# Kernel optimization log

Measured on AMD Instinct MI355X. Metric: run time of the kernel, lower is better.

## Reference

```python
import jax, jax.numpy as jnp
import numpy as np

# ---- static config (from init_kwargs) ----
SAMPLE_RATE = 2048.0
MAX_SHIFT = int(0.025 * SAMPLE_RATE)          # 51 samples
NUM_BINS = 16
FFTLENGTH = 1.0                               # chisq_kernel_length (s)
DF = 1.0 / FFTLENGTH
NUM_FREQS = int(FFTLENGTH * SAMPLE_RATE // 2 + 1)   # 1025 == rfft bins of 2048 samples
HIGHPASS = 32.0
CHISQ_PENALTY = 1.0
_freqs = np.arange(NUM_FREQS) / FFTLENGTH
MASK = _freqs >= HIGHPASS                     # static numpy bool mask

BATCH, CHANNELS, DIM = 256, 2, 2048


def setup_inputs() -> dict:
    key = jax.random.key(0)
    k1, k2 = jax.random.split(key)
    x_hat = jax.random.normal(k1, (BATCH, CHANNELS, DIM), dtype=jnp.float32)
    x = jax.random.normal(k2, (BATCH, CHANNELS, DIM), dtype=jnp.float32)
    return {"x_hat": x_hat, "x": x}


def _center(x):
    xmin = x.min(-1, keepdims=True)
    xmax = x.max(-1, keepdims=True)
    return 2 * (x - xmin) / (xmax - xmin) - 1


def _shifted_pearson(x, y, max_shift):
    # x, y: [B, C, T]; returns corr: [W, B, C] with W = 2*max_shift + 1
    b, c, t = x.shape
    num_windows = 2 * max_shift + 1
    xp = jnp.pad(x, ((0, 0), (0, 0), (max_shift, max_shift)))
    # window w, position i -> xp[..., i + w]  (same layout as torch unfold)
    idx = jnp.arange(num_windows)[:, None] + jnp.arange(t)[None, :]   # [W, T]
    xw = xp[:, :, idx]                                                # [B, C, W, T]
    xw = jnp.transpose(xw, (2, 0, 1, 3))                              # [W, B, C, T]
    xw = xw - xw.mean(-1, keepdims=True)
    yc = y - y.mean(-1, keepdims=True)
    corr = (xw * yc).sum(-1)
    norm = (xw ** 2).sum(-1) * (yc ** 2).sum(-1)
    return corr / jnp.sqrt(norm)


def _snr_integral(a, b):
    # |4 * a * conj(b) * df| cumulatively summed over frequency
    integrand = a * jnp.conj(b)
    return jnp.abs(4 * integrand * DF).cumsum(-1)


def _chisq(htilde, stilde):
    htilde = htilde[:, :, MASK]
    stilde = stilde[:, :, MASK]
    # partition frequencies by the template's own optimal-SNR integral
    si = _snr_integral(htilde, htilde)                    # [B, C, F]
    total = si[:, :, -1:]
    bins = (jnp.arange(NUM_BINS + 1, dtype=si.dtype) / NUM_BINS) * total  # [B, C, NB+1]
    search = jax.vmap(jax.vmap(lambda a, v: jnp.searchsorted(a, v, side="right")))
    edges = search(si, bins)
    edges = jnp.clip(edges, 0, si.shape[-1] - 1)
    qtilde = htilde / jnp.sqrt(total).astype(htilde.dtype)
    # SNR per bin of the normalized template against the strain
    si2 = _snr_integral(qtilde, stilde)                   # [B, C, F]
    total2 = si2[:, :, -1:]
    right = jnp.take_along_axis(si2, edges[:, :, 1:], axis=-1)
    left = jnp.take_along_axis(si2, edges[:, :, :-1], axis=-1)
    snr_per_bin = right - left                            # [B, C, NB]
    summand = (snr_per_bin - total2 / NUM_BINS) ** 2
    chisq = NUM_BINS * summand.sum(-1) / (NUM_BINS - 1)
    return total2[:, :, 0], chisq


def reference(x_hat, x):
    x_hat = _center(x_hat)
    corr = _shifted_pearson(x_hat, x, MAX_SHIFT)          # [W, B, C]
    corr = corr.max(0)                                    # [B, C]
    loss = (1 - corr) / (1 + corr)
    htilde = jnp.fft.rfft(x_hat, axis=-1) / SAMPLE_RATE   # [B, C, 1025] complex
    stilde = jnp.fft.rfft(x, axis=-1) / SAMPLE_RATE
    _, chisq = _chisq(htilde, stilde)
    chisq = chisq * CHISQ_PENALTY
    loss = loss * (1 + chisq ** 3) ** (1.0 / 6.0)
    return loss
```

## Files before the change

kernel.cpp:

```cpp
#include <hip/hip_runtime.h>
#include <math.h>

#define ROWS 512
#define DIM 2048
#define MS 51
#define NWIN 103
#define KMIN 32
#define NMASK 993
#define PHYS(i) ((i) + ((i) >> 5))

__global__ __launch_bounds__(256) void fused_mfl_kernel(
    const float* __restrict__ xhat, const float* __restrict__ x,
    float* __restrict__ out)
{
    const int r = blockIdx.x;
    const int t = threadIdx.x;
    const int lane = t & 63;
    const int wave = t >> 6;
    const float* xh = xhat + (size_t)r * DIM;
    const float* xr = x + (size_t)r * DIM;

    __shared__ float smem[9216];
    float* yh    = smem;
    float* yc    = smem + 2224;
    float* headS = smem + 4352;
    float* headQ = smem + 4404;
    float* tailS = smem + 4456;
    float* tailQ = smem + 4508;
    float2* A  = (float2*)smem;
    float2* Bb = (float2*)(smem + 4096);
    float2* TW = (float2*)(smem + 8192);
    float* siA = smem + 4096;
    float* siB = smem + 5120;

    __shared__ float red[32];
    __shared__ float sc[8];
    __shared__ int   edges[17];
    __shared__ float summ[16];
    __shared__ float wsum[4];

    float4 a0 = ((const float4*)xh)[2 * t];
    float4 a1 = ((const float4*)xh)[2 * t + 1];
    float4 b0 = ((const float4*)xr)[2 * t];
    float4 b1 = ((const float4*)xr)[2 * t + 1];
    float av[8] = {a0.x, a0.y, a0.z, a0.w, a1.x, a1.y, a1.z, a1.w};
    float bv[8] = {b0.x, b0.y, b0.z, b0.w, b1.x, b1.y, b1.z, b1.w};

#pragma unroll
    for (int k = 0; k < 2; ++k) {
        int u = t + 256 * k;
        float swv, cwv;
        sincosf((float)u * (-3.14159265358979323846f / 1024.0f), &swv, &cwv);
        TW[u] = make_float2(cwv, swv);
    }

    float mn = av[0], mx = av[0], sx = 0.f;
#pragma unroll
    for (int j = 0; j < 8; ++j) {
        mn = fminf(mn, av[j]); mx = fmaxf(mx, av[j]); sx += bv[j];
    }
#pragma unroll
    for (int d = 32; d; d >>= 1) {
        mn = fminf(mn, __shfl_down(mn, d));
        mx = fmaxf(mx, __shfl_down(mx, d));
        sx += __shfl_down(sx, d);
    }
    if (lane == 0) { red[wave] = mn; red[8 + wave] = mx; red[16 + wave] = sx; }
    __syncthreads();
    if (t == 0) {
        sc[0] = fminf(fminf(red[0], red[1]), fminf(red[2], red[3]));
        sc[1] = fmaxf(fmaxf(red[8], red[9]), fmaxf(red[10], red[11]));
        sc[2] = (red[16] + red[17] + red[18] + red[19]) * (1.0f / DIM);
    }
    __syncthreads();
    mn = sc[0]; mx = sc[1];
    const float mean = sc[2];
    const float scale = 2.0f / (mx - mn);

    float s1 = 0.f, s2 = 0.f, syy = 0.f;
    float yhv[8];
#pragma unroll
    for (int j = 0; j < 8; ++j) {
        float y = (av[j] - mn) * scale - 1.0f;
        float z = bv[j] - mean;
        yhv[j] = y;
        s1 += y; s2 += y * y; syy += z * z;
        int i = 8 * t + j;
        yh[PHYS(i + MS)] = y;
        yc[PHYS(i)] = z;
    }
    if (t < MS) { yh[PHYS(t)] = 0.f; yh[PHYS(t + MS + DIM)] = 0.f; }

#pragma unroll
    for (int d = 32; d; d >>= 1) {
        s1 += __shfl_down(s1, d); s2 += __shfl_down(s2, d); syy += __shfl_down(syy, d);
    }
    if (lane == 0) { red[wave] = s1; red[8 + wave] = s2; red[16 + wave] = syy; }
    __syncthreads();
    if (t == 0) {
        sc[3] = red[0] + red[1] + red[2] + red[3];
        sc[4] = red[8] + red[9] + red[10] + red[11];
        sc[5] = red[16] + red[17] + red[18] + red[19];
    }
    __syncthreads();
    const float S1 = sc[3], S2 = sc[4], Syy = sc[5];

    if (wave < 2) {
        float v = 0.f;
        if (lane >= 1 && lane <= MS)
            v = (wave == 0) ? yh[PHYS(MS + lane - 1)] : yh[PHYS(MS + DIM - lane)];
        float s = v, q = v * v;
#pragma unroll
        for (int d = 1; d < 64; d <<= 1) {
            float ys = __shfl_up(s, d);
            float yq = __shfl_up(q, d);
            if (lane >= d) { s += ys; q += yq; }
        }
        if (lane <= MS) {
            if (wave == 0) { headS[lane] = s; headQ[lane] = q; }
            else           { tailS[lane] = s; tailQ[lane] = q; }
        }
    }
    __syncthreads();

    float ycr[32];
#pragma unroll
    for (int j = 0; j < 32; ++j) ycr[j] = yc[PHYS(32 * lane + j)];

    const int c0 = 26 * wave;
    const int base0 = 32 * lane + c0;
    float wreg[32];
#pragma unroll
    for (int j = 0; j < 32; ++j) wreg[j] = yh[PHYS(base0 + j)];

    float cmax = -2.0f;
#pragma unroll
    for (int i = 0; i < 26; ++i) {
        float acc = 0.f;
#pragma unroll
        for (int j = 0; j < 32; ++j) acc += wreg[(i + j) & 31] * ycr[j];
#pragma unroll
        for (int d = 32; d; d >>= 1) acc += __shfl_down(acc, d);
        int c = c0 + i;
        if (lane == 0 && c < NWIN) {
            int off = c - MS;
            float sw, qw;
            if (off >= 0) { sw = S1 - headS[off]; qw = S2 - headQ[off]; }
            else          { sw = S1 - tailS[-off]; qw = S2 - tailQ[-off]; }
            float varw = qw - sw * sw * (1.0f / DIM);
            float corr = acc / sqrtf(varw * Syy);
            cmax = fmaxf(cmax, corr);
        }
        if (i < 25) wreg[i & 31] = yh[PHYS(base0 + 32 + i)];
    }
    if (lane == 0) red[wave] = cmax;
    __syncthreads();
    if (t == 0) {
        float m = fmaxf(fmaxf(red[0], red[1]), fmaxf(red[2], red[3]));
        sc[6] = (1.0f - m) / (1.0f + m);
    }
    __syncthreads();

#pragma unroll
    for (int j = 0; j < 8; ++j) {
        A[8 * t + j] = make_float2(yhv[j], bv[j]);
    }
    __syncthreads();

    float2 *S = A, *D = Bb;
#pragma unroll
    for (int stage = 0; stage < 5; ++stage) {
        const int s = 1 << (2 * stage);
#pragma unroll
        for (int k = 0; k < 2; ++k) {
            int q = t + 256 * k;
            int u = q & ~(s - 1);
            float2 x0 = S[q];
            float2 x1 = S[q + 512];
            float2 x2 = S[q + 1024];
            float2 x3 = S[q + 1536];
            float t0r = x0.x + x2.x, t0i = x0.y + x2.y;
            float t1r = x0.x - x2.x, t1i = x0.y - x2.y;
            float t2r = x1.x + x3.x, t2i = x1.y + x3.y;
            float d3r = x1.x - x3.x, d3i = x1.y - x3.y;
            float t3r = d3i, t3i = -d3r;
            float2 w1 = TW[u];
            float w2r = w1.x * w1.x - w1.y * w1.y, w2i = 2.f * w1.x * w1.y;
            float w3r = w2r * w1.x - w2i * w1.y,  w3i = w2r * w1.y + w2i * w1.x;
            float y0r = t0r + t2r, y0i = t0i + t2i;
            float a1r = t1r + t3r, a1i = t1i + t3i;
            float y1r = a1r * w1.x - a1i * w1.y, y1i = a1r * w1.y + a1i * w1.x;
            float a2r = t0r - t2r, a2i = t0i - t2i;
            float y2r = a2r * w2r - a2i * w2i, y2i = a2r * w2i + a2i * w2r;
            float a3r = t1r - t3r, a3i = t1i - t3i;
            float y3r = a3r * w3r - a3i * w3i, y3i = a3r * w3i + a3i * w3r;
            int base = q + 3 * u;
            D[base]         = make_float2(y0r, y0i);
            D[base + s]     = make_float2(y1r, y1i);
            D[base + 2 * s] = make_float2(y2r, y2i);
            D[base + 3 * s] = make_float2(y3r, y3i);
        }
        __syncthreads();
        float2* tmp = S; S = D; D = tmp;
    }
#pragma unroll
    for (int k = 0; k < 4; ++k) {
        int b = t + 256 * k;
        float2 a = S[b], c = S[b + 1024];
        D[b]        = make_float2(a.x + c.x, a.y + c.y);
        D[b + 1024] = make_float2(a.x - c.x, a.y - c.y);
    }
    __syncthreads();

    const float MSC = 0.5f * (1.0f / 2048.0f);
    float h[4], sg[4];
#pragma unroll
    for (int j = 0; j < 4; ++j) {
        int m = 4 * t + j;
        if (m < NMASK) {
            int f = m + KMIN;
            int g = 2048 - f;
            float2 zf = A[f];
            float2 zg = A[g];
            float hre = zf.x + zg.x, him = zf.y - zg.y;
            float sre = zf.y + zg.y, sim = zg.x - zf.x;
            h[j]  = sqrtf(hre * hre + him * him) * MSC;
            sg[j] = sqrtf(sre * sre + sim * sim) * MSC;
        } else { h[j] = 0.f; sg[j] = 0.f; }
    }

    float e0 = 4.f * h[0] * h[0];
    float e1 = e0 + 4.f * h[1] * h[1];
    float e2 = e1 + 4.f * h[2] * h[2];
    float e3 = e2 + 4.f * h[3] * h[3];
    float tot = e3;
    float inc = tot;
#pragma unroll
    for (int d = 1; d < 64; d <<= 1) {
        float y = __shfl_up(inc, d);
        if (lane >= d) inc += y;
    }
    if (lane == 63) wsum[wave] = inc;
    __syncthreads();
    float woff = 0.f;
    for (int w = 0; w < wave; ++w) woff += wsum[w];
    float pre = woff + inc - tot;
    siA[4 * t + 0] = pre + e0;
    siA[4 * t + 1] = pre + e1;
    siA[4 * t + 2] = pre + e2;
    siA[4 * t + 3] = pre + e3;
    __syncthreads();
    const float total = siA[NMASK - 1];

    const float q = 1.0f / sqrtf(total);
    float g0 = 4.f * h[0] * sg[0] * q;
    float g1 = g0 + 4.f * h[1] * sg[1] * q;
    float g2 = g1 + 4.f * h[2] * sg[2] * q;
    float g3 = g2 + 4.f * h[3] * sg[3] * q;
    float tot2l = g3;
    float inc2 = tot2l;
#pragma unroll
    for (int d = 1; d < 64; d <<= 1) {
        float y = __shfl_up(inc2, d);
        if (lane >= d) inc2 += y;
    }
    if (lane == 63) wsum[wave] = inc2;
    __syncthreads();
    float woff2 = 0.f;
    for (int w = 0; w < wave; ++w) woff2 += wsum[w];
    float pre2 = woff2 + inc2 - tot2l;
    siB[4 * t + 0] = pre2 + g0;
    siB[4 * t + 1] = pre2 + g1;
    siB[4 * t + 2] = pre2 + g2;
    siB[4 * t + 3] = pre2 + g3;
    __syncthreads();
    const float total2 = siB[NMASK - 1];

    if (t < 17) {
        float bin = ((float)t * (1.0f / 16.0f)) * total;
        int lo = 0, hi = NMASK;
        while (lo < hi) {
            int mid = (lo + hi) >> 1;
            if (siA[mid] <= bin) lo = mid + 1; else hi = mid;
        }
        edges[t] = (lo < NMASK - 1) ? lo : (NMASK - 1);
    }
    __syncthreads();

    if (t < 16) {
        float snr = siB[edges[t + 1]] - siB[edges[t]];
        float d = snr - total2 * (1.0f / 16.0f);
        summ[t] = d * d;
    }
    __syncthreads();
    if (t == 0) {
        float ssum = 0.f;
        for (int i = 0; i < 16; ++i) ssum += summ[i];
        float chisq = 16.0f * ssum / 15.0f;
        float c3 = chisq * chisq * chisq;
        out[r] = sc[6] * powf(1.0f + c3, 1.0f / 6.0f);
    }
}

extern "C" void kernel_launch(void* const* d_in, const int* in_sizes, int n_in,
                              void* d_out, int out_size, void* d_ws, size_t ws_size,
                              hipStream_t stream) {
    const float* xhat = (const float*)d_in[0];
    const float* x    = (const float*)d_in[1];
    float* out = (float*)d_out;
    (void)d_ws; (void)ws_size;

    fused_mfl_kernel<<<ROWS, 256, 0, stream>>>(xhat, x, out);
}
```

Baseline: 77.83 us.

## Use 512 threads per row, fuse final FFT stage into extraction, merge prefix scans

```diff
diff --git a/kernel.cpp b/kernel.cpp
--- a/kernel.cpp
+++ b/kernel.cpp
@@ -9,7 +9,7 @@
 #define NMASK 993
 #define PHYS(i) ((i) + ((i) >> 5))
 
-__global__ __launch_bounds__(256) void fused_mfl_kernel(
+__global__ __launch_bounds__(512) void fused_mfl_kernel(
     const float* __restrict__ xhat, const float* __restrict__ x,
     float* __restrict__ out)
 {
@@ -30,33 +30,29 @@
     float2* A  = (float2*)smem;
     float2* Bb = (float2*)(smem + 4096);
     float2* TW = (float2*)(smem + 8192);
-    float* siA = smem + 4096;
-    float* siB = smem + 5120;
+    float* siA  = smem;
+    float* siBr = smem + 1024;
 
     __shared__ float red[32];
     __shared__ float sc[8];
     __shared__ int   edges[17];
     __shared__ float summ[16];
-    __shared__ float wsum[4];
-
-    float4 a0 = ((const float4*)xh)[2 * t];
-    float4 a1 = ((const float4*)xh)[2 * t + 1];
-    float4 b0 = ((const float4*)xr)[2 * t];
-    float4 b1 = ((const float4*)xr)[2 * t + 1];
-    float av[8] = {a0.x, a0.y, a0.z, a0.w, a1.x, a1.y, a1.z, a1.w};
-    float bv[8] = {b0.x, b0.y, b0.z, b0.w, b1.x, b1.y, b1.z, b1.w};
-
-#pragma unroll
-    for (int k = 0; k < 2; ++k) {
-        int u = t + 256 * k;
+    __shared__ float wsA[8], wsB[8];
+
+    float4 a4 = ((const float4*)xh)[t];
+    float4 b4 = ((const float4*)xr)[t];
+    float av[4] = {a4.x, a4.y, a4.z, a4.w};
+    float bv[4] = {b4.x, b4.y, b4.z, b4.w};
+
+    {
         float swv, cwv;
-        sincosf((float)u * (-3.14159265358979323846f / 1024.0f), &swv, &cwv);
-        TW[u] = make_float2(cwv, swv);
+        sincosf((float)t * (-3.14159265358979323846f / 1024.0f), &swv, &cwv);
+        TW[t] = make_float2(cwv, swv);
     }
 
     float mn = av[0], mx = av[0], sx = 0.f;
 #pragma unroll
-    for (int j = 0; j < 8; ++j) {
+    for (int j = 0; j < 4; ++j) {
         mn = fminf(mn, av[j]); mx = fmaxf(mx, av[j]); sx += bv[j];
     }
 #pragma unroll
@@ -68,9 +64,11 @@
     if (lane == 0) { red[wave] = mn; red[8 + wave] = mx; red[16 + wave] = sx; }
     __syncthreads();
     if (t == 0) {
-        sc[0] = fminf(fminf(red[0], red[1]), fminf(red[2], red[3]));
-        sc[1] = fmaxf(fmaxf(red[8], red[9]), fmaxf(red[10], red[11]));
-        sc[2] = (red[16] + red[17] + red[18] + red[19]) * (1.0f / DIM);
+        float m0 = red[0], m1 = red[8], s = red[16];
+        for (int w = 1; w < 8; ++w) {
+            m0 = fminf(m0, red[w]); m1 = fmaxf(m1, red[8 + w]); s += red[16 + w];
+        }
+        sc[0] = m0; sc[1] = m1; sc[2] = s * (1.0f / DIM);
     }
     __syncthreads();
     mn = sc[0]; mx = sc[1];
@@ -78,14 +76,14 @@
     const float scale = 2.0f / (mx - mn);
 
     float s1 = 0.f, s2 = 0.f, syy = 0.f;
-    float yhv[8];
-#pragma unroll
-    for (int j = 0; j < 8; ++j) {
+    float yhv[4];
+#pragma unroll
+    for (int j = 0; j < 4; ++j) {
         float y = (av[j] - mn) * scale - 1.0f;
         float z = bv[j] - mean;
         yhv[j] = y;
         s1 += y; s2 += y * y; syy += z * z;
-        int i = 8 * t + j;
+        int i = 4 * t + j;
         yh[PHYS(i + MS)] = y;
         yc[PHYS(i)] = z;
     }
@@ -98,9 +96,9 @@
     if (lane == 0) { red[wave] = s1; red[8 + wave] = s2; red[16 + wave] = syy; }
     __syncthreads();
     if (t == 0) {
-        sc[3] = red[0] + red[1] + red[2] + red[3];
-        sc[4] = red[8] + red[9] + red[10] + red[11];
-        sc[5] = red[16] + red[17] + red[18] + red[19];
+        float p0 = 0.f, p1 = 0.f, p2 = 0.f;
+        for (int w = 0; w < 8; ++w) { p0 += red[w]; p1 += red[8 + w]; p2 += red[16 + w]; }
+        sc[3] = p0; sc[4] = p1; sc[5] = p2;
     }
     __syncthreads();
     const float S1 = sc[3], S2 = sc[4], Syy = sc[5];
@@ -127,7 +125,7 @@
 #pragma unroll
     for (int j = 0; j < 32; ++j) ycr[j] = yc[PHYS(32 * lane + j)];
 
-    const int c0 = 26 * wave;
+    const int c0 = 13 * wave;
     const int base0 = 32 * lane + c0;
     float wreg[32];
 #pragma unroll
@@ -135,7 +133,7 @@
 
     float cmax = -2.0f;
 #pragma unroll
-    for (int i = 0; i < 26; ++i) {
+    for (int i = 0; i < 13; ++i) {
         float acc = 0.f;
 #pragma unroll
         for (int j = 0; j < 32; ++j) acc += wreg[(i + j) & 31] * ycr[j];
@@ -151,19 +149,19 @@
             float corr = acc / sqrtf(varw * Syy);
             cmax = fmaxf(cmax, corr);
         }
-        if (i < 25) wreg[i & 31] = yh[PHYS(base0 + 32 + i)];
+        if (i < 12) wreg[i & 31] = yh[PHYS(base0 + 32 + i)];
     }
     if (lane == 0) red[wave] = cmax;
     __syncthreads();
     if (t == 0) {
-        float m = fmaxf(fmaxf(red[0], red[1]), fmaxf(red[2], red[3]));
+        float m = red[0];
+        for (int w = 1; w < 8; ++w) m = fmaxf(m, red[w]);
         sc[6] = (1.0f - m) / (1.0f + m);
     }
-    __syncthreads();
-
-#pragma unroll
-    for (int j = 0; j < 8; ++j) {
-        A[8 * t + j] = make_float2(yhv[j], bv[j]);
+
+#pragma unroll
+    for (int j = 0; j < 4; ++j) {
+        A[4 * t + j] = make_float2(yhv[j], bv[j]);
     }
     __syncthreads();
 
@@ -171,59 +169,56 @@
 #pragma unroll
     for (int stage = 0; stage < 5; ++stage) {
         const int s = 1 << (2 * stage);
-#pragma unroll
-        for (int k = 0; k < 2; ++k) {
-            int q = t + 256 * k;
-            int u = q & ~(s - 1);
-            float2 x0 = S[q];
-            float2 x1 = S[q + 512];
-            float2 x2 = S[q + 1024];
-            float2 x3 = S[q + 1536];
-            float t0r = x0.x + x2.x, t0i = x0.y + x2.y;
-            float t1r = x0.x - x2.x, t1i = x0.y - x2.y;
-            float t2r = x1.x + x3.x, t2i = x1.y + x3.y;
-            float d3r = x1.x - x3.x, d3i = x1.y - x3.y;
-            float t3r = d3i, t3i = -d3r;
-            float2 w1 = TW[u];
-            float w2r = w1.x * w1.x - w1.y * w1.y, w2i = 2.f * w1.x * w1.y;
-            float w3r = w2r * w1.x - w2i * w1.y,  w3i = w2r * w1.y + w2i * w1.x;
-            float y0r = t0r + t2r, y0i = t0i + t2i;
-            float a1r = t1r + t3r, a1i = t1i + t3i;
-            float y1r = a1r * w1.x - a1i * w1.y, y1i = a1r * w1.y + a1i * w1.x;
-            float a2r = t0r - t2r, a2i = t0i - t2i;
-            float y2r = a2r * w2r - a2i * w2i, y2i = a2r * w2i + a2i * w2r;
-            float a3r = t1r - t3r, a3i = t1i - t3i;
-            float y3r = a3r * w3r - a3i * w3i, y3i = a3r * w3i + a3i * w3r;
-            int base = q + 3 * u;
-            D[base]         = make_float2(y0r, y0i);
-            D[base + s]     = make_float2(y1r, y1i);
-            D[base + 2 * s] = make_float2(y2r, y2i);
-            D[base + 3 * s] = make_float2(y3r, y3i);
-        }
+        const int q = t;
+        const int u = q & ~(s - 1);
+        float2 x0 = S[q];
+        float2 x1 = S[q + 512];
+        float2 x2 = S[q + 1024];
+        float2 x3 = S[q + 1536];
+        float t0r = x0.x + x2.x, t0i = x0.y + x2.y;
+        float t1r = x0.x - x2.x, t1i = x0.y - x2.y;
+        float t2r = x1.x + x3.x, t2i = x1.y + x3.y;
+        float d3r = x1.x - x3.x, d3i = x1.y - x3.y;
+        float t3r = d3i, t3i = -d3r;
+        float2 w1 = TW[u];
+        float w2r = w1.x * w1.x - w1.y * w1.y, w2i = 2.f * w1.x * w1.y;
+        float w3r = w2r * w1.x - w2i * w1.y,  w3i = w2r * w1.y + w2i * w1.x;
+        float y0r = t0r + t2r, y0i = t0i + t2i;
+        float a1r = t1r + t3r, a1i = t1i + t3i;
+        float y1r = a1r * w1.x - a1i * w1.y, y1i = a1r * w1.y + a1i * w1.x;
+        float a2r = t0r - t2r, a2i = t0i - t2i;
+        float y2r = a2r * w2r - a2i * w2i, y2i = a2r * w2i + a2i * w2r;
+        float a3r = t1r - t3r, a3i = t1i - t3i;
+        float y3r = a3r * w3r - a3i * w3i, y3i = a3r * w3i + a3i * w3r;
+        int base = q + 3 * u;
+        D[base]         = make_float2(y0r, y0i);
+        D[base + s]     = make_float2(y1r, y1i);
+        D[base + 2 * s] = make_float2(y2r, y2i);
+        D[base + 3 * s] = make_float2(y3r, y3i);
         __syncthreads();
         float2* tmp = S; S = D; D = tmp;
     }
-#pragma unroll
-    for (int k = 0; k < 4; ++k) {
-        int b = t + 256 * k;
-        float2 a = S[b], c = S[b + 1024];
-        D[b]        = make_float2(a.x + c.x, a.y + c.y);
-        D[b + 1024] = make_float2(a.x - c.x, a.y - c.y);
-    }
-    __syncthreads();
 
     const float MSC = 0.5f * (1.0f / 2048.0f);
-    float h[4], sg[4];
-#pragma unroll
-    for (int j = 0; j < 4; ++j) {
-        int m = 4 * t + j;
+    float h[2], sg[2];
+#pragma unroll
+    for (int j = 0; j < 2; ++j) {
+        int m = 2 * t + j;
         if (m < NMASK) {
             int f = m + KMIN;
+            float zfr, zfi;
+            if (f < 1024) {
+                float2 p = S[f], q2 = S[f + 1024];
+                zfr = p.x + q2.x; zfi = p.y + q2.y;
+            } else {
+                float2 p = S[0], q2 = S[1024];
+                zfr = p.x - q2.x; zfi = p.y - q2.y;
+            }
             int g = 2048 - f;
-            float2 zf = A[f];
-            float2 zg = A[g];
-            float hre = zf.x + zg.x, him = zf.y - zg.y;
-            float sre = zf.y + zg.y, sim = zg.x - zf.x;
+            float2 p2 = S[g - 1024], q3 = S[g];
+            float zgr = p2.x - q3.x, zgi = p2.y - q3.y;
+            float hre = zfr + zgr, him = zfi - zgi;
+            float sre = zfi + zgi, sim = zgr - zfr;
             h[j]  = sqrtf(hre * hre + him * him) * MSC;
             sg[j] = sqrtf(sre * sre + sim * sim) * MSC;
         } else { h[j] = 0.f; sg[j] = 0.f; }
@@ -231,50 +226,30 @@
 
     float e0 = 4.f * h[0] * h[0];
     float e1 = e0 + 4.f * h[1] * h[1];
-    float e2 = e1 + 4.f * h[2] * h[2];
-    float e3 = e2 + 4.f * h[3] * h[3];
-    float tot = e3;
-    float inc = tot;
+    float g0 = 4.f * h[0] * sg[0];
+    float g1 = g0 + 4.f * h[1] * sg[1];
+    float totE = e1, totG = g1;
+    float incE = totE, incG = totG;
 #pragma unroll
     for (int d = 1; d < 64; d <<= 1) {
-        float y = __shfl_up(inc, d);
-        if (lane >= d) inc += y;
-    }
-    if (lane == 63) wsum[wave] = inc;
-    __syncthreads();
-    float woff = 0.f;
-    for (int w = 0; w < wave; ++w) woff += wsum[w];
-    float pre = woff + inc - tot;
-    siA[4 * t + 0] = pre + e0;
-    siA[4 * t + 1] = pre + e1;
-    siA[4 * t + 2] = pre + e2;
-    siA[4 * t + 3] = pre + e3;
-    __syncthreads();
-    const float total = siA[NMASK - 1];
-
-    const float q = 1.0f / sqrtf(total);
-    float g0 = 4.f * h[0] * sg[0] * q;
-    float g1 = g0 + 4.f * h[1] * sg[1] * q;
-    float g2 = g1 + 4.f * h[2] * sg[2] * q;
-    float g3 = g2 + 4.f * h[3] * sg[3] * q;
-    float tot2l = g3;
-    float inc2 = tot2l;
-#pragma unroll
-    for (int d = 1; d < 64; d <<= 1) {
-        float y = __shfl_up(inc2, d);
-        if (lane >= d) inc2 += y;
-    }
-    if (lane == 63) wsum[wave] = inc2;
-    __syncthreads();
-    float woff2 = 0.f;
-    for (int w = 0; w < wave; ++w) woff2 += wsum[w];
-    float pre2 = woff2 + inc2 - tot2l;
-    siB[4 * t + 0] = pre2 + g0;
-    siB[4 * t + 1] = pre2 + g1;
-    siB[4 * t + 2] = pre2 + g2;
-    siB[4 * t + 3] = pre2 + g3;
-    __syncthreads();
-    const float total2 = siB[NMASK - 1];
+        float yE = __shfl_up(incE, d);
+        float yG = __shfl_up(incG, d);
+        if (lane >= d) { incE += yE; incG += yG; }
+    }
+    if (lane == 63) { wsA[wave] = incE; wsB[wave] = incG; }
+    __syncthreads();
+    float offE = 0.f, offG = 0.f;
+    for (int w = 0; w < wave; ++w) { offE += wsA[w]; offG += wsB[w]; }
+    float preE = offE + incE - totE;
+    float preG = offG + incG - totG;
+    siA[2 * t]      = preE + e0;
+    siA[2 * t + 1]  = preE + e1;
+    siBr[2 * t]     = preG + g0;
+    siBr[2 * t + 1] = preG + g1;
+    __syncthreads();
+    const float total  = siA[NMASK - 1];
+    const float qf     = 1.0f / sqrtf(total);
+    const float total2 = siBr[NMASK - 1] * qf;
 
     if (t < 17) {
         float bin = ((float)t * (1.0f / 16.0f)) * total;
@@ -288,7 +263,7 @@
     __syncthreads();
 
     if (t < 16) {
-        float snr = siB[edges[t + 1]] - siB[edges[t]];
+        float snr = (siBr[edges[t + 1]] - siBr[edges[t]]) * qf;
         float d = snr - total2 * (1.0f / 16.0f);
         summ[t] = d * d;
     }
@@ -310,5 +285,5 @@
     float* out = (float*)d_out;
     (void)d_ws; (void)ws_size;
 
-    fused_mfl_kernel<<<ROWS, 256, 0, stream>>>(xhat, x, out);
+    fused_mfl_kernel<<<ROWS, 512, 0, stream>>>(xhat, x, out);
 }
```

New measurement: 73.22 us. 5.9% less time.
